# Performance work log

Measured on AMD Instinct MI355X. Metric: run time of the kernel, lower is better.

Reference implementation:

```python
import jax, jax.numpy as jnp
import numpy as np

WS = (8, 7, 7)      # init window_size
SS = (4, 3, 3)      # init shift_size
HEADS = 4
EPS = 1e-3          # keras LayerNormalization default epsilon


def get_window_size(x_size, window_size, shift_size):
    ws = list(window_size); ss = list(shift_size)
    for i in range(len(x_size)):
        if x_size[i] <= window_size[i]:
            ws[i] = x_size[i]; ss[i] = 0
    return tuple(ws), tuple(ss)


def rel_pos_index(wd, wh, ww):
    # Faithful copy of get_relative_position_index (incl. its meshgrid quirks).
    y_y, z_z, x_x = np.meshgrid(np.arange(ww), np.arange(wd), np.arange(wh))  # indexing='xy'
    coords = np.stack([z_z, y_y, x_x], 0).reshape(3, -1)
    rel = (coords[:, :, None] - coords[:, None, :]).transpose(1, 2, 0)
    z = (rel[:, :, 0] + wd - 1) * (2 * wh - 1) * (2 * ww - 1)
    x = (rel[:, :, 1] + wh - 1) * (2 * ww - 1)
    y = rel[:, :, 2] + ww - 1
    return z + x + y  # (N, N) int


def window_partition(x, ws):
    B, D, H, W, C = x.shape
    x = x.reshape(B, D // ws[0], ws[0], H // ws[1], ws[1], W // ws[2], ws[2], C)
    x = x.transpose(0, 1, 3, 5, 2, 4, 6, 7)
    return x.reshape(-1, ws[0] * ws[1] * ws[2], C)


def window_reverse(w, ws, B, D, H, W):
    x = w.reshape(B, D // ws[0], H // ws[1], W // ws[2], ws[0], ws[1], ws[2], -1)
    x = x.transpose(0, 1, 4, 2, 5, 3, 6, 7)
    return x.reshape(B, D, H, W, -1)


def _slices(L, w, s):
    return [slice(0, -w), slice(-w, -s), slice(-s, None)] if s > 0 else [slice(None)]


def compute_mask(D, H, W, ws, ss):
    img = np.zeros((1, D, H, W, 1), np.float32)
    cnt = 0
    for d in _slices(D, ws[0], ss[0]):
        for h in _slices(H, ws[1], ss[1]):
            for w in _slices(W, ws[2], ss[2]):
                img[:, d, h, w, :] = cnt; cnt += 1
    x = img.reshape(1, D // ws[0], ws[0], H // ws[1], ws[1], W // ws[2], ws[2], 1)
    mw = x.transpose(0, 1, 3, 5, 2, 4, 6, 7).reshape(-1, ws[0] * ws[1] * ws[2])
    am = mw[:, None, :] - mw[:, :, None]
    return jnp.asarray(np.where(am != 0, -100.0, 0.0).astype(np.float32))  # (nW, N, N)


def layernorm(x, g, b):
    m = jnp.mean(x, -1, keepdims=True)
    v = jnp.mean(jnp.square(x - m), -1, keepdims=True)
    return (x - m) * jax.lax.rsqrt(v + EPS) * g + b


def setup_inputs() -> dict:
    key = jax.random.key(0)
    ks = jax.random.split(key, 8)
    C = 128; Hd = 4 * C
    f = lambda k, sh: jax.random.normal(k, sh, jnp.float32) * 0.02
    tbl = (2 * WS[0] - 1) * (2 * WS[1] - 1) * (2 * WS[2] - 1)
    return dict(
        x=jax.random.normal(ks[0], (2, 8, 56, 56, C), jnp.float32),
        norm1_g=jnp.ones((C,), jnp.float32), norm1_b=jnp.zeros((C,), jnp.float32),
        qkv_w=f(ks[1], (C, 3 * C)), qkv_b=jnp.zeros((3 * C,), jnp.float32),
        proj_w=f(ks[2], (C, C)), proj_b=jnp.zeros((C,), jnp.float32),
        rpb=f(ks[3], (tbl, HEADS)),
        norm2_g=jnp.ones((C,), jnp.float32), norm2_b=jnp.zeros((C,), jnp.float32),
        fc1_w=f(ks[4], (C, Hd)), fc1_b=jnp.zeros((Hd,), jnp.float32),
        fc2_w=f(ks[5], (Hd, C)), fc2_b=jnp.zeros((C,), jnp.float32),
    )


def reference(x, norm1_g, norm1_b, qkv_w, qkv_b, proj_w, proj_b, rpb,
              norm2_g, norm2_b, fc1_w, fc1_b, fc2_w, fc2_b):
    B, D, H, W, C = x.shape
    ws, ss = get_window_size((D, H, W), WS, SS)
    shortcut = x
    xn = layernorm(x, norm1_g, norm1_b)
    # dims divisible by window -> no padding branch
    shifted = jnp.roll(xn, (-ss[0], -ss[1], -ss[2]), (1, 2, 3)) if any(ss) else xn
    mask = compute_mask(D, H, W, ws, ss) if any(ss) else None

    xw = window_partition(shifted, ws)          # (B*nW, N, C)
    Bn, N, _ = xw.shape
    hd = C // HEADS
    scale = hd ** -0.5

    qkv = (xw @ qkv_w + qkv_b).reshape(Bn, N, 3, HEADS, hd).transpose(2, 0, 3, 1, 4)
    q, k, v = qkv[0] * scale, qkv[1], qkv[2]    # (Bn, heads, N, hd)
    attn = jnp.einsum('bhnd,bhmd->bhnm', q, k)
    idx = rel_pos_index(*WS)[:N, :N]
    bias = rpb[idx].transpose(2, 0, 1)          # (heads, N, N)
    attn = attn + bias[None]
    if mask is not None:
        nW = mask.shape[0]
        attn = attn.reshape(Bn // nW, nW, HEADS, N, N) + mask[None, :, None]
        attn = attn.reshape(-1, HEADS, N, N)
    attn = jax.nn.softmax(attn, axis=-1)
    out = jnp.einsum('bhnm,bhmd->bhnd', attn, v).transpose(0, 2, 1, 3).reshape(Bn, N, C)
    out = out @ proj_w + proj_b

    xr = window_reverse(out, ws, B, D, H, W)
    if any(ss):
        xr = jnp.roll(xr, ss, (1, 2, 3))
    x = shortcut + xr

    xn2 = layernorm(x, norm2_g, norm2_b)
    h = jax.nn.gelu(xn2 @ fc1_w + fc1_b, approximate=False)
    return x + (h @ fc2_w + fc2_b)
```

## Files before the change

kernel.cpp:

```cpp
#include <hip/hip_runtime.h>
#include <math.h>

#define TOK    50176
#define CH     128
#define NWIN   128
#define NTOK   392
#define NHEADS 4
#define QSCALE 0.17677669529663687f
#define LNEPS  1e-3f

typedef unsigned short u16;
typedef unsigned int   u32;
typedef u16   u16x4  __attribute__((ext_vector_type(4)));
typedef u16   u16x8  __attribute__((ext_vector_type(8)));
typedef short s16x8  __attribute__((ext_vector_type(8)));
typedef float f32x4  __attribute__((ext_vector_type(4)));

__device__ __forceinline__ float bf2f(u16 u) {
    return __uint_as_float(((u32)u) << 16);
}
__device__ __forceinline__ u16 f2bf(float f) {
    u32 u = __float_as_uint(f);
    return (u16)((u + 0x7fffu + ((u >> 16) & 1u)) >> 16);
}
__device__ __forceinline__ f32x4 mfma16(s16x8 a, s16x8 b, f32x4 c) {
    return __builtin_amdgcn_mfma_f32_16x16x32_bf16(a, b, c, 0, 0, 0);
}

__device__ __forceinline__ int src_index(int m) {
    int b = m / NTOK, t = m - b * NTOK;
    int batch = b >> 6, wIdx = b & 63;
    int bh = wIdx >> 3, bw = wIdx & 7;
    int d = t / 49, rem = t - d * 49;
    int h7 = rem / 7, w7 = rem - h7 * 7;
    int h = bh * 7 + h7 + 3; if (h >= 56) h -= 56;
    int w = bw * 7 + w7 + 3; if (w >= 56) w -= 56;
    return ((batch * 8 + d) * 56 + h) * 56 + w;
}

__global__ __launch_bounds__(256) void convT(
    const float* __restrict__ src, u16* __restrict__ dst,
    int K, int N, int scaleN)
{
    __shared__ float t[32][33];
    int n0 = blockIdx.x * 32, k0 = blockIdx.y * 32;
    int tx = threadIdx.x & 31, ty = threadIdx.x >> 5;
    #pragma unroll
    for (int r = 0; r < 4; ++r)
        t[ty + r * 8][tx] = src[(size_t)(k0 + ty + r * 8) * N + n0 + tx];
    __syncthreads();
    #pragma unroll
    for (int r = 0; r < 4; ++r) {
        int n = n0 + ty + r * 8;
        float sc = (n < scaleN) ? QSCALE : 1.f;
        dst[(size_t)n * K + k0 + tx] = f2bf(t[tx][ty + r * 8] * sc);
    }
}

__global__ __launch_bounds__(128) void ln_kernel(
    const float* __restrict__ xin,
    const float* __restrict__ g, const float* __restrict__ bta,
    u16* __restrict__ out)
{
    int m = blockIdx.x, c = threadIdx.x;
    float v = xin[(size_t)src_index(m) * CH + c];
    float s1 = v, s2 = v * v;
    #pragma unroll
    for (int o = 32; o; o >>= 1) { s1 += __shfl_xor(s1, o); s2 += __shfl_xor(s2, o); }
    __shared__ float ps[2][2];
    int w = c >> 6;
    if ((c & 63) == 0) { ps[w][0] = s1; ps[w][1] = s2; }
    __syncthreads();
    s1 = ps[0][0] + ps[1][0];
    s2 = ps[0][1] + ps[1][1];
    float mean = s1 * (1.f / CH);
    float var  = s2 * (1.f / CH) - mean * mean;
    float r = rsqrtf(var + LNEPS);
    out[(size_t)m * CH + c] = f2bf((v - mean) * r * g[c] + bta[c]);
}

template<int EPI, int KTOT>
__global__ __launch_bounds__(512, 6) void gemm_mfma(
    const u16* __restrict__ A, const u16* __restrict__ W,
    const float* __restrict__ bias, void* __restrict__ outp,
    int Nn, const float* __restrict__ resid, const u16* __restrict__ residb,
    const float* __restrict__ lng, const float* __restrict__ lnb,
    u16* __restrict__ ln_out)
{
    __shared__ u16 As[4][64][32];
    __shared__ u16 Bs[4][128][32];
    __shared__ float lnred[2][4][16][2];

    int tid = threadIdx.x, w = tid >> 6, l = tid & 63;
    int c16 = l & 15, g4 = l >> 4;
    int m0 = blockIdx.y * 64, n0 = blockIdx.x * 128;
    int wm = w & 3, wn = w >> 2;
    const int NCH = KTOT / 128;

    f32x4 acc[4] = {};
    u16x8 va[2], vb[4];

    #pragma unroll
    for (int p = 0; p < 2; ++p) {
        int e = tid + p * 512, row = e >> 4, c8 = e & 15;
        va[p] = *(const u16x8*)&A[(size_t)(m0 + row) * KTOT + c8 * 8];
    }
    #pragma unroll
    for (int p = 0; p < 4; ++p) {
        int e = tid + p * 512, row = e >> 4, c8 = e & 15;
        vb[p] = *(const u16x8*)&W[(size_t)(n0 + row) * KTOT + c8 * 8];
    }
    for (int ch = 0; ch < NCH; ++ch) {
        #pragma unroll
        for (int p = 0; p < 2; ++p) {
            int e = tid + p * 512, row = e >> 4, c8 = e & 15;
            *(u16x8*)&As[c8 >> 2][row][(c8 & 3) * 8] = va[p];
        }
        #pragma unroll
        for (int p = 0; p < 4; ++p) {
            int e = tid + p * 512, row = e >> 4, c8 = e & 15;
            *(u16x8*)&Bs[c8 >> 2][row][(c8 & 3) * 8] = vb[p];
        }
        __syncthreads();
        if (ch + 1 < NCH) {
            #pragma unroll
            for (int p = 0; p < 2; ++p) {
                int e = tid + p * 512, row = e >> 4, c8 = e & 15;
                va[p] = *(const u16x8*)&A[(size_t)(m0 + row) * KTOT + (ch + 1) * 128 + c8 * 8];
            }
            #pragma unroll
            for (int p = 0; p < 4; ++p) {
                int e = tid + p * 512, row = e >> 4, c8 = e & 15;
                vb[p] = *(const u16x8*)&W[(size_t)(n0 + row) * KTOT + (ch + 1) * 128 + c8 * 8];
            }
        }
        #pragma unroll
        for (int kc = 0; kc < 4; ++kc) {
            s16x8 af = __builtin_bit_cast(s16x8,
                *(const u16x8*)&As[kc][wm * 16 + c16][g4 * 8]);
            #pragma unroll
            for (int ni = 0; ni < 4; ++ni) {
                s16x8 bf = __builtin_bit_cast(s16x8,
                    *(const u16x8*)&Bs[kc][wn * 64 + ni * 16 + c16][g4 * 8]);
                acc[ni] = mfma16(af, bf, acc[ni]);
            }
        }
        if (ch + 1 < NCH) __syncthreads();
    }

    if (EPI == 2) {
        float psum[4], psq[4];
        int dstl[4];
        #pragma unroll
        for (int r = 0; r < 4; ++r) {
            int m = m0 + wm * 16 + g4 * 4 + r;
            int dst = src_index(m);
            dstl[r] = dst;
            float s = 0.f, q = 0.f;
            #pragma unroll
            for (int ni = 0; ni < 4; ++ni) {
                int col = wn * 64 + ni * 16 + c16;
                float v = acc[ni][r] + bias[col] + resid[(size_t)dst * CH + col];
                acc[ni][r] = v;
                s += v; q += v * v;
            }
            psum[r] = s; psq[r] = q;
        }
        #pragma unroll
        for (int o = 1; o <= 8; o <<= 1)
            #pragma unroll
            for (int r = 0; r < 4; ++r) {
                psum[r] += __shfl_xor(psum[r], o);
                psq[r]  += __shfl_xor(psq[r], o);
            }
        if (c16 == 0) {
            #pragma unroll
            for (int r = 0; r < 4; ++r) {
                int rl = g4 * 4 + r;
                lnred[wn][wm][rl][0] = psum[r];
                lnred[wn][wm][rl][1] = psq[r];
            }
        }
        __syncthreads();
        float gl[4], bl[4];
        #pragma unroll
        for (int ni = 0; ni < 4; ++ni) {
            int col = wn * 64 + ni * 16 + c16;
            gl[ni] = lng[col]; bl[ni] = lnb[col];
        }
        #pragma unroll
        for (int r = 0; r < 4; ++r) {
            int rl = g4 * 4 + r;
            float s = lnred[0][wm][rl][0] + lnred[1][wm][rl][0];
            float q = lnred[0][wm][rl][1] + lnred[1][wm][rl][1];
            float mean = s * (1.f / CH);
            float var  = q * (1.f / CH) - mean * mean;
            float rstd = rsqrtf(var + LNEPS);
            int dst = dstl[r];
            #pragma unroll
            for (int ni = 0; ni < 4; ++ni) {
                int col = wn * 64 + ni * 16 + c16;
                float v = acc[ni][r];
                ((u16*)outp)[(size_t)dst * CH + col] = f2bf(v);
                ln_out[(size_t)dst * CH + col] = f2bf((v - mean) * rstd * gl[ni] + bl[ni]);
            }
        }
    } else {
        #pragma unroll
        for (int r = 0; r < 4; ++r) {
            int m = m0 + wm * 16 + g4 * 4 + r;
            #pragma unroll
            for (int ni = 0; ni < 4; ++ni) {
                int col = n0 + wn * 64 + ni * 16 + c16;
                float v = acc[ni][r];
                if (EPI == 1) {
                    v += bias[col] * (col < 128 ? QSCALE : 1.f);
                    ((u16*)outp)[(size_t)m * Nn + col] = f2bf(v);
                } else if (EPI == 3) {
                    v += bias[col];
                    v = 0.5f * v * (1.f + erff(v * 0.70710678118654752f));
                    ((u16*)outp)[(size_t)m * Nn + col] = f2bf(v);
                } else {
                    v += bias[col];
                    ((float*)outp)[(size_t)m * CH + col]
                        = v + bf2f(residb[(size_t)m * CH + col]);
                }
            }
        }
    }
}

__global__ __launch_bounds__(64) void bias_k(
    const float* __restrict__ rpb, float* __restrict__ biasT2)
{
    int nt = blockIdx.x;
    int t  = blockIdx.y;
    int hw = blockIdx.z;
    int l  = threadIdx.x;
    int head = hw >> 2, wt = hw & 3;
    int bh7 = wt >> 1, bw7 = wt & 1;
    int j = nt * 16 + (l & 15);
    int rb = t * 16 + (l >> 4) * 4;
    f32x4 outv;
    #pragma unroll
    for (int r = 0; r < 4; ++r) {
        int i = rb + r; if (i > NTOK - 1) i = NTOK - 1;
        float v;
        if (j >= NTOK) v = -100.f;
        else {
            int di = i / 49, ri = i - di * 49, hi = ri / 7, wi = ri - hi * 7;
            int dj = j / 49, rj = j - dj * 49, hj = rj / 7, wj = rj - hj * 7;
            int bidx = (di - dj + 7) * 169 + (hi - hj + 6) * 13 + (wi - wj + 6);
            v = rpb[bidx * NHEADS + head];
            int regi = (bh7 ? (hi < 4 ? 1 : 2) : 0) * 3 + (bw7 ? (wi < 4 ? 1 : 2) : 0);
            int regj = (bh7 ? (hj < 4 ? 1 : 2) : 0) * 3 + (bw7 ? (wj < 4 ? 1 : 2) : 0);
            if (regi != regj) v -= 100.f;
        }
        outv[r] = v;
    }
    *(f32x4*)&biasT2[((((size_t)hw * 25 + t) * 26 + nt) << 8) + (l << 2)] = outv;
}

__global__ __launch_bounds__(512, 4) void attn_mfma(
    const u16* __restrict__ Qb, const float* __restrict__ biasT2,
    u16* __restrict__ O)
{
    __shared__ u16 Vt[32][420];
    __shared__ u16 Pst[8][3][16][40];

    int bid = blockIdx.x;
    int win = bid >> 2, head = bid & 3;
    int tid = threadIdx.x, w = tid >> 6, l = tid & 63;
    int c16 = l & 15, g4 = l >> 4;

    const size_t qbase = (size_t)win * NTOK * 384;
    for (int e = tid; e < 1600; e += 512) {
        int j = e >> 2, d0 = (e & 3) * 8;
        u16x8 vv = {0, 0, 0, 0, 0, 0, 0, 0};
        if (j < NTOK)
            vv = *(const u16x8*)&Qb[qbase + (size_t)j * 384 + 256 + head * 32 + d0];
        #pragma unroll
        for (int i = 0; i < 8; ++i) Vt[d0 + i][j] = vv[i];
    }
    if (tid < 32 * 16) Vt[tid >> 4][400 + (tid & 15)] = 0;
    __syncthreads();

    int wIdx = win & 63;
    int wt = (((wIdx >> 3) == 7) ? 2 : 0) + (((wIdx & 7) == 7) ? 1 : 0);
    const float* bt = biasT2 + (((size_t)(head * 4 + wt) * 25 * 26) << 8) + (l << 2);
    const u16* kroot = Qb + qbase + 128 + head * 32 + g4 * 8;
    u16 (*myPA)[40] = Pst[w][0];
    u16 (*myPB)[40] = Pst[w][1];
    u16 (*myPC)[40] = Pst[w][2];

    {
        int tA = w, tB = w + 8, tC = w + 16;
        s16x8 qfragA = __builtin_bit_cast(s16x8,
            *(const u16x8*)&Qb[qbase + (size_t)(tA * 16 + c16) * 384 + head * 32 + g4 * 8]);
        s16x8 qfragB = __builtin_bit_cast(s16x8,
            *(const u16x8*)&Qb[qbase + (size_t)(tB * 16 + c16) * 384 + head * 32 + g4 * 8]);
        s16x8 qfragC = __builtin_bit_cast(s16x8,
            *(const u16x8*)&Qb[qbase + (size_t)(tC * 16 + c16) * 384 + head * 32 + g4 * 8]);
        const float* bttA = bt + (((size_t)tA * 26) << 8);
        const float* bttB = bt + (((size_t)tB * 26) << 8);
        const float* bttC = bt + (((size_t)tC * 26) << 8);

        float l4A[4] = {0.f,0.f,0.f,0.f}, l4B[4] = {0.f,0.f,0.f,0.f}, l4C[4] = {0.f,0.f,0.f,0.f};
        f32x4 oaccA0 = {0.f,0.f,0.f,0.f}, oaccA1 = {0.f,0.f,0.f,0.f};
        f32x4 oaccB0 = {0.f,0.f,0.f,0.f}, oaccB1 = {0.f,0.f,0.f,0.f};
        f32x4 oaccC0 = {0.f,0.f,0.f,0.f}, oaccC1 = {0.f,0.f,0.f,0.f};

        for (int jb = 0; jb < 13; ++jb) {
            int kr0 = jb * 32 + c16;      if (kr0 > NTOK - 1) kr0 = NTOK - 1;
            int kr1 = jb * 32 + 16 + c16; if (kr1 > NTOK - 1) kr1 = NTOK - 1;
            s16x8 kf0 = __builtin_bit_cast(s16x8, *(const u16x8*)&kroot[(size_t)kr0 * 384]);
            s16x8 kf1 = __builtin_bit_cast(s16x8, *(const u16x8*)&kroot[(size_t)kr1 * 384]);
            f32x4 sA0 = mfma16(qfragA, kf0, *(const f32x4*)(bttA + (((size_t)(jb*2+0)) << 8)));
            f32x4 sA1 = mfma16(qfragA, kf1, *(const f32x4*)(bttA + (((size_t)(jb*2+1)) << 8)));
            f32x4 sB0 = mfma16(qfragB, kf0, *(const f32x4*)(bttB + (((size_t)(jb*2+0)) << 8)));
            f32x4 sB1 = mfma16(qfragB, kf1, *(const f32x4*)(bttB + (((size_t)(jb*2+1)) << 8)));
            f32x4 sC0 = mfma16(qfragC, kf0, *(const f32x4*)(bttC + (((size_t)(jb*2+0)) << 8)));
            f32x4 sC1 = mfma16(qfragC, kf1, *(const f32x4*)(bttC + (((size_t)(jb*2+1)) << 8)));
            #pragma unroll
            for (int r = 0; r < 4; ++r) {
                float p0 = exp2f(sA0[r] * 1.44269504f);
                float p1 = exp2f(sA1[r] * 1.44269504f);
                l4A[r] += p0 + p1;
                myPA[g4 * 4 + r][c16]      = f2bf(p0);
                myPA[g4 * 4 + r][16 + c16] = f2bf(p1);
            }
            #pragma unroll
            for (int r = 0; r < 4; ++r) {
                float p0 = exp2f(sB0[r] * 1.44269504f);
                float p1 = exp2f(sB1[r] * 1.44269504f);
                l4B[r] += p0 + p1;
                myPB[g4 * 4 + r][c16]      = f2bf(p0);
                myPB[g4 * 4 + r][16 + c16] = f2bf(p1);
            }
            #pragma unroll
            for (int r = 0; r < 4; ++r) {
                float p0 = exp2f(sC0[r] * 1.44269504f);
                float p1 = exp2f(sC1[r] * 1.44269504f);
                l4C[r] += p0 + p1;
                myPC[g4 * 4 + r][c16]      = f2bf(p0);
                myPC[g4 * 4 + r][16 + c16] = f2bf(p1);
            }
            s16x8 paA = __builtin_bit_cast(s16x8, *(const u16x8*)&myPA[c16][g4 * 8]);
            s16x8 paB = __builtin_bit_cast(s16x8, *(const u16x8*)&myPB[c16][g4 * 8]);
            s16x8 paC = __builtin_bit_cast(s16x8, *(const u16x8*)&myPC[c16][g4 * 8]);
            s16x8 vb0 = __builtin_bit_cast(s16x8, *(const u16x8*)&Vt[c16][jb * 32 + g4 * 8]);
            s16x8 vb1 = __builtin_bit_cast(s16x8, *(const u16x8*)&Vt[16 + c16][jb * 32 + g4 * 8]);
            oaccA0 = mfma16(paA, vb0, oaccA0);
            oaccA1 = mfma16(paA, vb1, oaccA1);
            oaccB0 = mfma16(paB, vb0, oaccB0);
            oaccB1 = mfma16(paB, vb1, oaccB1);
            oaccC0 = mfma16(paC, vb0, oaccC0);
            oaccC1 = mfma16(paC, vb1, oaccC1);
        }

        #pragma unroll
        for (int r = 0; r < 4; ++r) {
            #pragma unroll
            for (int o = 1; o <= 8; o <<= 1) {
                l4A[r] += __shfl_xor(l4A[r], o);
                l4B[r] += __shfl_xor(l4B[r], o);
                l4C[r] += __shfl_xor(l4C[r], o);
            }
            l4A[r] = 1.f / l4A[r];
            l4B[r] = 1.f / l4B[r];
            l4C[r] = 1.f / l4C[r];
        }
        #pragma unroll
        for (int r = 0; r < 4; ++r) {
            int qA = tA * 16 + g4 * 4 + r;
            int qB = tB * 16 + g4 * 4 + r;
            int qC = tC * 16 + g4 * 4 + r;
            size_t oA = ((size_t)(win * NTOK + qA)) * CH + head * 32 + c16;
            size_t oB = ((size_t)(win * NTOK + qB)) * CH + head * 32 + c16;
            size_t oC = ((size_t)(win * NTOK + qC)) * CH + head * 32 + c16;
            O[oA]      = f2bf(oaccA0[r] * l4A[r]);
            O[oA + 16] = f2bf(oaccA1[r] * l4A[r]);
            O[oB]      = f2bf(oaccB0[r] * l4B[r]);
            O[oB + 16] = f2bf(oaccB1[r] * l4B[r]);
            O[oC]      = f2bf(oaccC0[r] * l4C[r]);
            O[oC + 16] = f2bf(oaccC1[r] * l4C[r]);
        }
    }

    if (w == 0) {
        int t = 24;
        int row0 = t * 16;
        int qr = row0 + c16; if (qr > NTOK - 1) qr = NTOK - 1;
        s16x8 afrag = __builtin_bit_cast(s16x8,
            *(const u16x8*)&Qb[qbase + (size_t)qr * 384 + head * 32 + g4 * 8]);
        const float* btt = bt + (((size_t)t * 26) << 8);

        float l4[4] = {0.f, 0.f, 0.f, 0.f};
        f32x4 oacc[2] = {{0.f,0.f,0.f,0.f},{0.f,0.f,0.f,0.f}};

        for (int jb = 0; jb < 13; ++jb) {
            f32x4 s[2];
            #pragma unroll
            for (int kk = 0; kk < 2; ++kk) {
                f32x4 cb = *(const f32x4*)(btt + (((size_t)(jb * 2 + kk)) << 8));
                int kr = jb * 32 + kk * 16 + c16;
                if (kr > NTOK - 1) kr = NTOK - 1;
                s16x8 bfrag = __builtin_bit_cast(s16x8,
                    *(const u16x8*)&kroot[(size_t)kr * 384]);
                s[kk] = mfma16(afrag, bfrag, cb);
            }
            #pragma unroll
            for (int kk = 0; kk < 2; ++kk)
                #pragma unroll
                for (int r = 0; r < 4; ++r) {
                    float p = exp2f(s[kk][r] * 1.44269504f);
                    l4[r] += p;
                    myPA[g4 * 4 + r][kk * 16 + c16] = f2bf(p);
                }
            s16x8 pa = __builtin_bit_cast(s16x8, *(const u16x8*)&myPA[c16][g4 * 8]);
            #pragma unroll
            for (int nd = 0; nd < 2; ++nd) {
                s16x8 vb = __builtin_bit_cast(s16x8,
                    *(const u16x8*)&Vt[nd * 16 + c16][jb * 32 + g4 * 8]);
                oacc[nd] = mfma16(pa, vb, oacc[nd]);
            }
        }

        #pragma unroll
        for (int r = 0; r < 4; ++r) {
            #pragma unroll
            for (int o = 1; o <= 8; o <<= 1)
                l4[r] += __shfl_xor(l4[r], o);
            l4[r] = 1.f / l4[r];
        }
        #pragma unroll
        for (int nd = 0; nd < 2; ++nd)
            #pragma unroll
            for (int r = 0; r < 4; ++r) {
                int qrow = row0 + g4 * 4 + r;
                if (qrow < NTOK)
                    O[((size_t)(win * NTOK + qrow)) * CH + head * 32 + nd * 16 + c16]
                        = f2bf(oacc[nd][r] * l4[r]);
            }
    }
}

extern "C" void kernel_launch(void* const* d_in, const int* in_sizes, int n_in,
                              void* d_out, int out_size, void* d_ws, size_t ws_size,
                              hipStream_t stream) {
    const float* x      = (const float*)d_in[0];
    const float* n1g    = (const float*)d_in[1];
    const float* n1b    = (const float*)d_in[2];
    const float* qkv_w  = (const float*)d_in[3];
    const float* qkv_b  = (const float*)d_in[4];
    const float* proj_w = (const float*)d_in[5];
    const float* proj_b = (const float*)d_in[6];
    const float* rpb    = (const float*)d_in[7];
    const float* n2g    = (const float*)d_in[8];
    const float* n2b    = (const float*)d_in[9];
    const float* fc1_w  = (const float*)d_in[10];
    const float* fc1_b  = (const float*)d_in[11];
    const float* fc2_w  = (const float*)d_in[12];
    const float* fc2_b  = (const float*)d_in[13];
    float* out = (float*)d_out;

    char* ws = (char*)d_ws;
    size_t off = 0;
    u16* A_bf  = (u16*)(ws + off);  off += (size_t)TOK * 128 * 2;
    u16* Qb_bf = (u16*)(ws + off);  off += (size_t)TOK * 384 * 2;
    u16* O_bf  = (u16*)(ws + off);  off += (size_t)TOK * 128 * 2;
    u16* R_bf  = (u16*)(ws + off);  off += (size_t)TOK * 128 * 2;
    u16* qkvT  = (u16*)(ws + off);  off += 384 * 128 * 2;
    u16* projT = (u16*)(ws + off);  off += 128 * 128 * 2;
    u16* fc1T  = (u16*)(ws + off);  off += 512 * 128 * 2;
    u16* fc2T  = (u16*)(ws + off);  off += 128 * 512 * 2;
    u16* H_bf  = Qb_bf;
    float* biasT2 = (float*)A_bf;

    hipLaunchKernelGGL(convT, dim3(384/32, 128/32), dim3(256), 0, stream, qkv_w,  qkvT, 128, 384, 128);
    hipLaunchKernelGGL(convT, dim3(128/32, 128/32), dim3(256), 0, stream, proj_w, projT, 128, 128, 0);
    hipLaunchKernelGGL(convT, dim3(512/32, 128/32), dim3(256), 0, stream, fc1_w,  fc1T, 128, 512, 0);
    hipLaunchKernelGGL(convT, dim3(128/32, 512/32), dim3(256), 0, stream, fc2_w,  fc2T, 512, 128, 0);
    hipLaunchKernelGGL(ln_kernel, dim3(TOK), dim3(128), 0, stream, x, n1g, n1b, A_bf);
    hipLaunchKernelGGL((gemm_mfma<1, 128>), dim3(3, TOK/64), dim3(512), 0, stream,
                       A_bf, qkvT, qkv_b, Qb_bf, 384, nullptr, nullptr, nullptr, nullptr, nullptr);
    hipLaunchKernelGGL(bias_k, dim3(26, 25, 16), dim3(64), 0, stream, rpb, biasT2);
    hipLaunchKernelGGL(attn_mfma, dim3(NWIN * NHEADS), dim3(512), 0, stream,
                       Qb_bf, biasT2, O_bf);
    hipLaunchKernelGGL((gemm_mfma<2, 128>), dim3(1, TOK/64), dim3(512), 0, stream,
                       O_bf, projT, proj_b, R_bf, 128, x, nullptr, n2g, n2b, A_bf);
    hipLaunchKernelGGL((gemm_mfma<3, 128>), dim3(4, TOK/64), dim3(512), 0, stream,
                       A_bf, fc1T, fc1_b, H_bf, 512, nullptr, nullptr, nullptr, nullptr, nullptr);
    hipLaunchKernelGGL((gemm_mfma<4, 512>), dim3(1, TOK/64), dim3(512), 0, stream,
                       H_bf, fc2T, fc2_b, out, 128, nullptr, R_bf, nullptr, nullptr, nullptr);
}
```

Before: 163.4 us.

## Fuse fc1+GELU and fc2 GEMMs into one MLP kernel keeping hidden in LDS

Replaces the separate fc1 (with GELU) and fc2 GEMM launches with a single kernel. Each 64-row tile computes a 128-wide hidden chunk, stores it as bf16 in shared memory, and immediately accumulates it into the fc2 output. This removes the global-memory write and re-read of the 50176x512 hidden activation and one launch. In exchange the kernel is serialized per chunk with more barriers, the weights are reloaded by every block, and occupancy is lower (launch bounds 2) with only 784 blocks.

```diff
diff --git a/kernel.cpp b/kernel.cpp
--- a/kernel.cpp
+++ b/kernel.cpp
@@ -83,7 +83,7 @@
 __global__ __launch_bounds__(512, 6) void gemm_mfma(
     const u16* __restrict__ A, const u16* __restrict__ W,
     const float* __restrict__ bias, void* __restrict__ outp,
-    int Nn, const float* __restrict__ resid, const u16* __restrict__ residb,
+    int Nn, const float* __restrict__ resid,
     const float* __restrict__ lng, const float* __restrict__ lnb,
     u16* __restrict__ ln_out)
 {
@@ -212,20 +212,100 @@
             #pragma unroll
             for (int ni = 0; ni < 4; ++ni) {
                 int col = n0 + wn * 64 + ni * 16 + c16;
-                float v = acc[ni][r];
-                if (EPI == 1) {
-                    v += bias[col] * (col < 128 ? QSCALE : 1.f);
-                    ((u16*)outp)[(size_t)m * Nn + col] = f2bf(v);
-                } else if (EPI == 3) {
-                    v += bias[col];
-                    v = 0.5f * v * (1.f + erff(v * 0.70710678118654752f));
-                    ((u16*)outp)[(size_t)m * Nn + col] = f2bf(v);
-                } else {
-                    v += bias[col];
-                    ((float*)outp)[(size_t)m * CH + col]
-                        = v + bf2f(residb[(size_t)m * CH + col]);
-                }
-            }
+                float v = acc[ni][r] + bias[col] * (col < 128 ? QSCALE : 1.f);
+                ((u16*)outp)[(size_t)m * Nn + col] = f2bf(v);
+            }
+        }
+    }
+}
+
+__global__ __launch_bounds__(512, 2) void mlp_fused(
+    const u16* __restrict__ A, const u16* __restrict__ W1,
+    const float* __restrict__ b1, const u16* __restrict__ W2,
+    const float* __restrict__ b2, const u16* __restrict__ residb,
+    float* __restrict__ outp)
+{
+    __shared__ u16 As[4][64][32];
+    __shared__ u16 Bs[4][128][32];
+    __shared__ u16 Hs[4][64][40];
+
+    int tid = threadIdx.x, w = tid >> 6, l = tid & 63;
+    int c16 = l & 15, g4 = l >> 4;
+    int m0 = blockIdx.x * 64;
+    int wm = w & 3, wn = w >> 2;
+
+    #pragma unroll
+    for (int p = 0; p < 2; ++p) {
+        int e = tid + p * 512, row = e >> 4, c8 = e & 15;
+        u16x8 v = *(const u16x8*)&A[(size_t)(m0 + row) * 128 + c8 * 8];
+        *(u16x8*)&As[c8 >> 2][row][(c8 & 3) * 8] = v;
+    }
+
+    f32x4 acc2[4] = {};
+    for (int ch = 0; ch < 4; ++ch) {
+        #pragma unroll
+        for (int p = 0; p < 4; ++p) {
+            int e = tid + p * 512, row = e >> 4, c8 = e & 15;
+            u16x8 v = *(const u16x8*)&W1[(size_t)(ch * 128 + row) * 128 + c8 * 8];
+            *(u16x8*)&Bs[c8 >> 2][row][(c8 & 3) * 8] = v;
+        }
+        __syncthreads();
+
+        f32x4 hacc[4] = {};
+        #pragma unroll
+        for (int kc = 0; kc < 4; ++kc) {
+            s16x8 af = __builtin_bit_cast(s16x8,
+                *(const u16x8*)&As[kc][wm * 16 + c16][g4 * 8]);
+            #pragma unroll
+            for (int ni = 0; ni < 4; ++ni) {
+                s16x8 bf = __builtin_bit_cast(s16x8,
+                    *(const u16x8*)&Bs[kc][wn * 64 + ni * 16 + c16][g4 * 8]);
+                hacc[ni] = mfma16(af, bf, hacc[ni]);
+            }
+        }
+        #pragma unroll
+        for (int r = 0; r < 4; ++r) {
+            int row = wm * 16 + g4 * 4 + r;
+            #pragma unroll
+            for (int ni = 0; ni < 4; ++ni) {
+                int col = wn * 64 + ni * 16 + c16;
+                float v = hacc[ni][r] + b1[ch * 128 + col];
+                v = 0.5f * v * (1.f + erff(v * 0.70710678118654752f));
+                Hs[col >> 5][row][col & 31] = f2bf(v);
+            }
+        }
+        __syncthreads();
+
+        #pragma unroll
+        for (int p = 0; p < 4; ++p) {
+            int e = tid + p * 512, row = e >> 4, c8 = e & 15;
+            u16x8 v = *(const u16x8*)&W2[(size_t)row * 512 + ch * 128 + c8 * 8];
+            *(u16x8*)&Bs[c8 >> 2][row][(c8 & 3) * 8] = v;
+        }
+        __syncthreads();
+
+        #pragma unroll
+        for (int kc = 0; kc < 4; ++kc) {
+            s16x8 af = __builtin_bit_cast(s16x8,
+                *(const u16x8*)&Hs[kc][wm * 16 + c16][g4 * 8]);
+            #pragma unroll
+            for (int ni = 0; ni < 4; ++ni) {
+                s16x8 bf = __builtin_bit_cast(s16x8,
+                    *(const u16x8*)&Bs[kc][wn * 64 + ni * 16 + c16][g4 * 8]);
+                acc2[ni] = mfma16(af, bf, acc2[ni]);
+            }
+        }
+        __syncthreads();
+    }
+
+    #pragma unroll
+    for (int r = 0; r < 4; ++r) {
+        int m = m0 + wm * 16 + g4 * 4 + r;
+        #pragma unroll
+        for (int ni = 0; ni < 4; ++ni) {
+            int col = wn * 64 + ni * 16 + c16;
+            float v = acc2[ni][r] + b2[col];
+            outp[(size_t)m * CH + col] = v + bf2f(residb[(size_t)m * CH + col]);
         }
     }
 }
@@ -474,7 +554,6 @@
     u16* projT = (u16*)(ws + off);  off += 128 * 128 * 2;
     u16* fc1T  = (u16*)(ws + off);  off += 512 * 128 * 2;
     u16* fc2T  = (u16*)(ws + off);  off += 128 * 512 * 2;
-    u16* H_bf  = Qb_bf;
     float* biasT2 = (float*)A_bf;
 
     hipLaunchKernelGGL(convT, dim3(384/32, 128/32), dim3(256), 0, stream, qkv_w,  qkvT, 128, 384, 128);
@@ -483,14 +562,12 @@
     hipLaunchKernelGGL(convT, dim3(128/32, 512/32), dim3(256), 0, stream, fc2_w,  fc2T, 512, 128, 0);
     hipLaunchKernelGGL(ln_kernel, dim3(TOK), dim3(128), 0, stream, x, n1g, n1b, A_bf);
     hipLaunchKernelGGL((gemm_mfma<1, 128>), dim3(3, TOK/64), dim3(512), 0, stream,
-                       A_bf, qkvT, qkv_b, Qb_bf, 384, nullptr, nullptr, nullptr, nullptr, nullptr);
+                       A_bf, qkvT, qkv_b, Qb_bf, 384, nullptr, nullptr, nullptr, nullptr);
     hipLaunchKernelGGL(bias_k, dim3(26, 25, 16), dim3(64), 0, stream, rpb, biasT2);
     hipLaunchKernelGGL(attn_mfma, dim3(NWIN * NHEADS), dim3(512), 0, stream,
                        Qb_bf, biasT2, O_bf);
     hipLaunchKernelGGL((gemm_mfma<2, 128>), dim3(1, TOK/64), dim3(512), 0, stream,
-                       O_bf, projT, proj_b, R_bf, 128, x, nullptr, n2g, n2b, A_bf);
-    hipLaunchKernelGGL((gemm_mfma<3, 128>), dim3(4, TOK/64), dim3(512), 0, stream,
-                       A_bf, fc1T, fc1_b, H_bf, 512, nullptr, nullptr, nullptr, nullptr, nullptr);
-    hipLaunchKernelGGL((gemm_mfma<4, 512>), dim3(1, TOK/64), dim3(512), 0, stream,
-                       H_bf, fc2T, fc2_b, out, 128, nullptr, R_bf, nullptr, nullptr, nullptr);
-}
+                       O_bf, projT, proj_b, R_bf, 128, x, n2g, n2b, A_bf);
+    hipLaunchKernelGGL(mlp_fused, dim3(TOK/64), dim3(512), 0, stream,
+                       A_bf, fc1T, fc1_b, fc2T, fc2_b, R_bf, out);
+}
```

After: 162.9 us. No clear change (-0.3%).
